# Kernel optimization log

Measured on AMD Instinct MI355X. Metric: run time of the kernel, lower is better.

Reference implementation:

```python
import jax, jax.numpy as jnp
import numpy as np

B, P, L1, D = 64, 16, 16, 1024  # images, people/img, object slots/img (slot0=no-object), feat dim
SP = 32   # flattened spatial (Conv_spatial output channels)
PROJ = 512
ACT = 29


def setup_inputs() -> dict:
    key = jax.random.key(0)
    ks = jax.random.split(key, 16)
    rn = lambda k, s, sc=1.0: jax.random.normal(k, s, dtype=jnp.float32) * sc
    w = 0.02  # weight init scale
    return {
        "people": rn(ks[0], (B, P, D)),
        "objects": rn(ks[1], (B, L1, D)),
        "context": rn(ks[2], (B, D)),
        "spatial": rn(ks[3], (B, P * L1, SP)),
        "Wvis_w": rn(ks[4], (3 * D, PROJ), w), "Wvis_b": jnp.zeros((PROJ,), jnp.float32),
        "Wspat_w": rn(ks[5], (SP, PROJ), w), "Wspat_b": jnp.zeros((PROJ,), jnp.float32),
        "Wip_w": rn(ks[6], (PROJ, 1), w), "Wip_b": jnp.zeros((1,), jnp.float32),
        "Wref_w": rn(ks[7], (PROJ, ACT), w), "Wref_b": jnp.zeros((ACT,), jnp.float32),
        "Watt_w": rn(ks[8], (PROJ, ACT), w), "Watt_b": jnp.zeros((ACT,), jnp.float32),
        "Woh_w": rn(ks[9], (D, D), w), "Woh_b": jnp.zeros((D,), jnp.float32),
        "Who_w": rn(ks[10], (D, D), w), "Who_b": jnp.zeros((D,), jnp.float32),
        "Wg_w": rn(ks[11], (2 * D, ACT), w), "Wg_b": jnp.zeros((ACT,), jnp.float32),
    }


def reference(people, objects, context, spatial,
              Wvis_w, Wvis_b, Wspat_w, Wspat_b, Wip_w, Wip_b,
              Wref_w, Wref_b, Watt_w, Watt_b,
              Woh_w, Woh_b, Who_w, Who_b, Wg_w, Wg_b):
    Bn, Pn, Dn = people.shape
    L = objects.shape[1]
    C = Bn * Pn * L

    # --- ROI.pairing: all (person, object-slot) pairs + image context -> [C, 3D]
    pe = jnp.broadcast_to(people[:, :, None, :], (Bn, Pn, L, Dn))
    ob = jnp.broadcast_to(objects[:, None, :, :], (Bn, Pn, L, Dn))
    cx = jnp.broadcast_to(context[:, None, None, :], (Bn, Pn, L, Dn))
    pairs = jnp.concatenate([pe, ob, cx], axis=-1).reshape(C, 3 * Dn)

    # --- attention / visual projection heads
    a_ho = jax.nn.relu(spatial.reshape(C, -1) @ Wspat_w + Wspat_b)   # W_Spat
    f_vis = jax.nn.relu(pairs @ Wvis_w + Wvis_b)                     # W_vis
    f_ref = f_vis * a_ho
    i_ho = f_ref @ Wip_w + Wip_b                                     # [C,1]
    interaction_prob = jax.nn.sigmoid(i_ho)
    p_ref = f_ref @ Wref_w + Wref_b                                  # [C,29]
    p_att = a_ho @ Watt_w + Watt_b                                   # [C,29]

    # --- graph message passing: adjacency = interaction probs, skipping slot 0 (no-object)
    adj = interaction_prob.reshape(Bn, Pn, L)[:, :, 1:]              # [B,P,O]
    oh = jax.nn.relu(objects[:, 1:] @ Woh_w + Woh_b)                 # W_oh on objects
    ho = jax.nn.relu(people @ Who_w + Who_b)                         # W_ho on people
    people_r = people + jnp.einsum('bpo,bod->bpd', adj, oh)
    objects_r = objects[:, 1:] + jnp.einsum('bpo,bpd->bod', adj, ho)
    objects_full = jnp.concatenate([objects[:, :1], objects_r], axis=1)  # re-attach no-object slot

    # --- refined all-pairs concat -> W_graph
    pe_r = jnp.broadcast_to(people_r[:, :, None, :], (Bn, Pn, L, Dn))
    ob_r = jnp.broadcast_to(objects_full[:, None, :, :], (Bn, Pn, L, Dn))
    pairs_g = jnp.concatenate([pe_r, ob_r], axis=-1).reshape(C, 2 * Dn)
    p_graph = pairs_g @ Wg_w + Wg_b                                  # [C,29]

    return (i_ho, p_ref, p_att, p_graph)
```

## Files before the change

kernel.cpp:

```cpp
#include <hip/hip_runtime.h>


typedef unsigned short u16;
typedef short s16x8 __attribute__((ext_vector_type(8)));
typedef float f32x4 __attribute__((ext_vector_type(4)));

__device__ __forceinline__ u16 f2b(float f) {
    union { float f; unsigned int i; } v; v.f = f;
    unsigned int r = (v.i + 0x7fffu + ((v.i >> 16) & 1u)) >> 16;
    return (u16)r;
}
__device__ __forceinline__ float b2f(u16 u) {
    union { float f; unsigned int i; } v; v.i = ((unsigned int)u) << 16; return v.f;
}
__device__ __forceinline__ unsigned int pack2(float x, float y) {
    return (unsigned int)f2b(x) | ((unsigned int)f2b(y) << 16);
}

#define OFF_WSPATT 0u
#define OFF_WREFT  32768u
#define OFF_WATTT  65536u
#define OFF_WGT    98304u
#define OFF_PP     229376u
#define OFF_PO     1277952u
#define OFF_PC     2326528u
#define OFF_ADJ    2392064u
#define OFF_HP     2457600u
#define OFF_HOF    2588672u
#define OFF_YH     2719744u
#define OFF_ZO     2850816u
#define ZERO_OFF   2457600u
#define ZERO_LEN   516096u
#define OFF_WVIST2 2973696u
#define OFF_WHOT2  6119424u
#define OFF_WOHT2  8216576u
#define OFF_PEOB   10313728u
#define OFF_OBJB   12410880u
#define OFF_CTXB   14508032u
#define OFF_SPATB  14639104u

__global__ __launch_bounds__(256) void prep_all(
    const float* __restrict__ people, const float* __restrict__ objects,
    const float* __restrict__ context, const float* __restrict__ spatial,
    const float* __restrict__ Wvis, const float* __restrict__ Who,
    const float* __restrict__ Woh, const float* __restrict__ Wspat,
    const float* __restrict__ Wref, const float* __restrict__ Watt,
    const float* __restrict__ Wg,
    u16* __restrict__ peoB, u16* __restrict__ objB, u16* __restrict__ ctxB,
    u16* __restrict__ spatB, u16* __restrict__ WvisT, u16* __restrict__ WhoT,
    u16* __restrict__ WohT, u16* __restrict__ WspatT, u16* __restrict__ WrefT,
    u16* __restrict__ WattT, u16* __restrict__ WgT)
{
    __shared__ float S[64][65];
    int bid = blockIdx.x, t = threadIdx.x;
    if (bid < 896) {
        const float* src; u16* dst; int N, K, kt, nt;
        int tb = bid;
        if (tb < 256)      { src = Who;  dst = WhoT;  K = 1024; N = 1024; kt = tb >> 4; nt = tb & 15; }
        else if (tb < 512) { tb -= 256; src = Woh;  dst = WohT;  K = 1024; N = 1024; kt = tb >> 4; nt = tb & 15; }
        else               { tb -= 512; src = Wvis; dst = WvisT; K = 3072; N = 512;  kt = tb >> 3; nt = tb & 7; }
        int k0 = kt * 64, n0 = nt * 64;
        int tx = t & 63, ty = t >> 6;
#pragma unroll
        for (int i = 0; i < 16; i++)
            S[ty + 4 * i][tx] = src[(size_t)(k0 + ty + 4 * i) * N + n0 + tx];
        __syncthreads();
#pragma unroll
        for (int i = 0; i < 16; i++)
            dst[(size_t)(n0 + ty + 4 * i) * K + k0 + tx] = f2b(S[tx][ty + 4 * i]);
        return;
    }
    int g = (bid - 896) * 256 + t;
    const int gsz = 512 * 256;
    for (int i = g; i < 524288; i += gsz) {
        float2 v = ((const float2*)people)[i];
        ((unsigned int*)peoB)[i] = pack2(v.x, v.y);
    }
    for (int i = g; i < 524288; i += gsz) {
        float2 v = ((const float2*)objects)[i];
        ((unsigned int*)objB)[i] = pack2(v.x, v.y);
    }
    for (int i = g; i < 32768; i += gsz) {
        float2 v = ((const float2*)context)[i];
        ((unsigned int*)ctxB)[i] = pack2(v.x, v.y);
    }
    for (int i = g; i < 262144; i += gsz) {
        float2 v = ((const float2*)spatial)[i];
        ((unsigned int*)spatB)[i] = pack2(v.x, v.y);
    }
    for (int i = g; i < 512 * 32; i += gsz) {
        int n = i >> 5, k = i & 31;
        WspatT[i] = f2b(Wspat[k * 512 + n]);
    }
    for (int i = g; i < 32 * 512; i += gsz) {
        int n = i >> 9, k = i & 511;
        WrefT[i] = (n < 29) ? f2b(Wref[k * 29 + n]) : (u16)0;
        WattT[i] = (n < 29) ? f2b(Watt[k * 29 + n]) : (u16)0;
    }
    for (int i = g; i < 32 * 2048; i += gsz) {
        int n = i >> 11, k = i & 2047;
        WgT[i] = (n < 29) ? f2b(Wg[k * 29 + n]) : (u16)0;
    }
}

__global__ __launch_bounds__(256) void fused_gemms(
    const u16* __restrict__ peoB, const u16* __restrict__ objB,
    const u16* __restrict__ ctxB, const u16* __restrict__ WvisT,
    const u16* __restrict__ WhoT, const float* __restrict__ Who_b,
    const u16* __restrict__ WohT, const float* __restrict__ Woh_b,
    const u16* __restrict__ WgT,
    u16* __restrict__ Pp, u16* __restrict__ Po, u16* __restrict__ Pc,
    float* __restrict__ Yh, float* __restrict__ Zo,
    float* __restrict__ Hp, float* __restrict__ HoF)
{
    __shared__ u16 T[128][72];
    int bid = blockIdx.x;
    int t = threadIdx.x;
    int lane = t & 63, w = t >> 6;
    int l16 = lane & 15, q = lane >> 4;
    int wy = w >> 1, wx = w & 1;

    if (bid < 264) {
        int bx = bid & 7, ty = bid >> 3;
        const u16* A; u16* outB; int koff, bm;
        if (ty < 16)      { A = peoB; outB = Pp; koff = 0;    bm = ty * 64; }
        else if (ty < 32) { A = objB; outB = Po; koff = 1024; bm = (ty - 16) * 64; }
        else              { A = ctxB; outB = Pc; koff = 2048; bm = 0; }
        int bn = bx * 64;

        const u16* ap0 = A + (size_t)(bm + wy * 32 + l16) * 1024 + q * 8;
        const u16* ap1 = ap0 + (size_t)16 * 1024;
        const u16* bp0 = WvisT + (size_t)(bn + wx * 32 + l16) * 3072 + koff + q * 8;
        const u16* bp1 = bp0 + (size_t)16 * 3072;

        f32x4 acc00 = {0,0,0,0}, acc01 = {0,0,0,0}, acc10 = {0,0,0,0}, acc11 = {0,0,0,0};
        s16x8 ca0 = *(const s16x8*)ap0,        ca1 = *(const s16x8*)ap1;
        s16x8 cb0 = *(const s16x8*)bp0,        cb1 = *(const s16x8*)bp1;
        s16x8 na0 = *(const s16x8*)(ap0 + 32), na1 = *(const s16x8*)(ap1 + 32);
        s16x8 nb0 = *(const s16x8*)(bp0 + 32), nb1 = *(const s16x8*)(bp1 + 32);
        ap0 += 64; ap1 += 64; bp0 += 64; bp1 += 64;
        for (int it = 0; it < 30; it++) {
            s16x8 ta0 = *(const s16x8*)ap0, ta1 = *(const s16x8*)ap1;
            s16x8 tb0 = *(const s16x8*)bp0, tb1 = *(const s16x8*)bp1;
            ap0 += 32; ap1 += 32; bp0 += 32; bp1 += 32;
            acc00 = __builtin_amdgcn_mfma_f32_16x16x32_bf16(ca0, cb0, acc00, 0, 0, 0);
            acc01 = __builtin_amdgcn_mfma_f32_16x16x32_bf16(ca0, cb1, acc01, 0, 0, 0);
            acc10 = __builtin_amdgcn_mfma_f32_16x16x32_bf16(ca1, cb0, acc10, 0, 0, 0);
            acc11 = __builtin_amdgcn_mfma_f32_16x16x32_bf16(ca1, cb1, acc11, 0, 0, 0);
            ca0 = na0; ca1 = na1; cb0 = nb0; cb1 = nb1;
            na0 = ta0; na1 = ta1; nb0 = tb0; nb1 = tb1;
        }
        acc00 = __builtin_amdgcn_mfma_f32_16x16x32_bf16(ca0, cb0, acc00, 0, 0, 0);
        acc01 = __builtin_amdgcn_mfma_f32_16x16x32_bf16(ca0, cb1, acc01, 0, 0, 0);
        acc10 = __builtin_amdgcn_mfma_f32_16x16x32_bf16(ca1, cb0, acc10, 0, 0, 0);
        acc11 = __builtin_amdgcn_mfma_f32_16x16x32_bf16(ca1, cb1, acc11, 0, 0, 0);
        acc00 = __builtin_amdgcn_mfma_f32_16x16x32_bf16(na0, nb0, acc00, 0, 0, 0);
        acc01 = __builtin_amdgcn_mfma_f32_16x16x32_bf16(na0, nb1, acc01, 0, 0, 0);
        acc10 = __builtin_amdgcn_mfma_f32_16x16x32_bf16(na1, nb0, acc10, 0, 0, 0);
        acc11 = __builtin_amdgcn_mfma_f32_16x16x32_bf16(na1, nb1, acc11, 0, 0, 0);

        f32x4 accs[2][2] = {{acc00, acc01}, {acc10, acc11}};
#pragma unroll
        for (int ii = 0; ii < 2; ii++)
#pragma unroll
            for (int jj = 0; jj < 2; jj++) {
                int col = bn + wx * 32 + jj * 16 + l16;
#pragma unroll
                for (int r = 0; r < 4; r++) {
                    int row = bm + wy * 32 + ii * 16 + q * 4 + r;
                    outB[(size_t)row * 512 + col] = f2b(accs[ii][jj][r]);
                }
            }
    } else if (bid < 520) {
        int r3 = bid - 264;
        int z = r3 >> 7; r3 &= 127;
        int rt = r3 >> 4, nbt = r3 & 15;
        const u16* A    = z ? objB : peoB;
        const u16* W1T  = z ? WohT : WhoT;
        const float* bb = z ? Woh_b : Who_b;
        const u16* Wg2  = z ? WgT : WgT + 1024;
        float* U        = z ? Zo : Yh;
        int m0 = rt * 128, nb = nbt * 64;

        const u16* ap[4];
        int rb = m0 + wy * 64;
#pragma unroll
        for (int i = 0; i < 4; i++) {
            int rr = rb + i * 16 + l16;
            if (z) { int rc = rr < 960 ? rr : 959; rr = (rc / 15) * 16 + (rc % 15) + 1; }
            ap[i] = A + (size_t)rr * 1024 + q * 8;
        }
        const u16* bp0 = W1T + (size_t)(nb + wx * 32 + l16) * 1024 + q * 8;
        const u16* bp1 = bp0 + (size_t)16 * 1024;

        f32x4 acc[4][2] = {};
        s16x8 ca[4], na[4];
#pragma unroll
        for (int i = 0; i < 4; i++) {
            ca[i] = *(const s16x8*)ap[i];
            na[i] = *(const s16x8*)(ap[i] + 32);
            ap[i] += 64;
        }
        s16x8 cb0 = *(const s16x8*)bp0, nb0 = *(const s16x8*)(bp0 + 32);
        s16x8 cb1 = *(const s16x8*)bp1, nb1 = *(const s16x8*)(bp1 + 32);
        bp0 += 64; bp1 += 64;
        for (int it = 0; it < 30; it++) {
            s16x8 ta[4], tb0, tb1;
#pragma unroll
            for (int i = 0; i < 4; i++) { ta[i] = *(const s16x8*)ap[i]; ap[i] += 32; }
            tb0 = *(const s16x8*)bp0; bp0 += 32;
            tb1 = *(const s16x8*)bp1; bp1 += 32;
#pragma unroll
            for (int i = 0; i < 4; i++) {
                acc[i][0] = __builtin_amdgcn_mfma_f32_16x16x32_bf16(ca[i], cb0, acc[i][0], 0, 0, 0);
                acc[i][1] = __builtin_amdgcn_mfma_f32_16x16x32_bf16(ca[i], cb1, acc[i][1], 0, 0, 0);
            }
#pragma unroll
            for (int i = 0; i < 4; i++) { ca[i] = na[i]; na[i] = ta[i]; }
            cb0 = nb0; nb0 = tb0; cb1 = nb1; nb1 = tb1;
        }
#pragma unroll
        for (int i = 0; i < 4; i++) {
            acc[i][0] = __builtin_amdgcn_mfma_f32_16x16x32_bf16(ca[i], cb0, acc[i][0], 0, 0, 0);
            acc[i][1] = __builtin_amdgcn_mfma_f32_16x16x32_bf16(ca[i], cb1, acc[i][1], 0, 0, 0);
        }
#pragma unroll
        for (int i = 0; i < 4; i++) {
            acc[i][0] = __builtin_amdgcn_mfma_f32_16x16x32_bf16(na[i], nb0, acc[i][0], 0, 0, 0);
            acc[i][1] = __builtin_amdgcn_mfma_f32_16x16x32_bf16(na[i], nb1, acc[i][1], 0, 0, 0);
        }

#pragma unroll
        for (int i = 0; i < 4; i++)
#pragma unroll
            for (int j = 0; j < 2; j++) {
                int col = wx * 32 + j * 16 + l16;
                float bv = bb[nb + col];
#pragma unroll
                for (int r = 0; r < 4; r++) {
                    float v = acc[i][j][r] + bv;
                    T[wy * 64 + i * 16 + q * 4 + r][col] = f2b(fmaxf(v, 0.f));
                }
            }
        __syncthreads();

        f32x4 s2[2][2] = {};
#pragma unroll
        for (int kk = 0; kk < 64; kk += 32) {
            s16x8 b20 = *(const s16x8*)(Wg2 + (size_t)l16 * 2048 + nb + kk + q * 8);
            s16x8 b21 = *(const s16x8*)(Wg2 + (size_t)(16 + l16) * 2048 + nb + kk + q * 8);
#pragma unroll
            for (int f = 0; f < 2; f++) {
                s16x8 a2 = *(const s16x8*)(&T[w * 32 + f * 16 + l16][kk + q * 8]);
                s2[f][0] = __builtin_amdgcn_mfma_f32_16x16x32_bf16(a2, b20, s2[f][0], 0, 0, 0);
                s2[f][1] = __builtin_amdgcn_mfma_f32_16x16x32_bf16(a2, b21, s2[f][1], 0, 0, 0);
            }
        }
#pragma unroll
        for (int f = 0; f < 2; f++)
#pragma unroll
            for (int r = 0; r < 4; r++) {
                int row = m0 + w * 32 + f * 16 + q * 4 + r;
                if (!z || row < 960) {
                    atomicAdd(&U[(size_t)row * 32 + l16], s2[f][0][r]);
                    atomicAdd(&U[(size_t)row * 32 + 16 + l16], s2[f][1][r]);
                }
            }
    } else {
        int r3 = bid - 520;
        int bx = r3 & 7, by = (r3 >> 3) & 7, z = r3 >> 6;
        const u16* A  = z ? objB : peoB;
        const u16* BT = z ? WgT + 1024 : WgT;
        float* outF   = z ? HoF : Hp;
        int bm = bx * 128 + w * 32;
        int kb = by * 128;
        const u16* ap0 = A + (size_t)(bm + l16) * 1024 + kb + q * 8;
        const u16* ap1 = A + (size_t)(bm + 16 + l16) * 1024 + kb + q * 8;
        const u16* bp0 = BT + (size_t)l16 * 2048 + kb + q * 8;
        const u16* bp1 = BT + (size_t)(16 + l16) * 2048 + kb + q * 8;
        f32x4 acc00 = {0,0,0,0}, acc01 = {0,0,0,0}, acc10 = {0,0,0,0}, acc11 = {0,0,0,0};
        s16x8 ca0 = *(const s16x8*)ap0,        ca1 = *(const s16x8*)ap1;
        s16x8 cb0 = *(const s16x8*)bp0,        cb1 = *(const s16x8*)bp1;
        s16x8 na0 = *(const s16x8*)(ap0 + 32), na1 = *(const s16x8*)(ap1 + 32);
        s16x8 nb0 = *(const s16x8*)(bp0 + 32), nb1 = *(const s16x8*)(bp1 + 32);
        ap0 += 64; ap1 += 64; bp0 += 64; bp1 += 64;
#pragma unroll
        for (int it = 0; it < 2; it++) {
            s16x8 ta0 = *(const s16x8*)ap0, ta1 = *(const s16x8*)ap1;
            s16x8 tb0 = *(const s16x8*)bp0, tb1 = *(const s16x8*)bp1;
            ap0 += 32; ap1 += 32; bp0 += 32; bp1 += 32;
            acc00 = __builtin_amdgcn_mfma_f32_16x16x32_bf16(ca0, cb0, acc00, 0, 0, 0);
            acc01 = __builtin_amdgcn_mfma_f32_16x16x32_bf16(ca0, cb1, acc01, 0, 0, 0);
            acc10 = __builtin_amdgcn_mfma_f32_16x16x32_bf16(ca1, cb0, acc10, 0, 0, 0);
            acc11 = __builtin_amdgcn_mfma_f32_16x16x32_bf16(ca1, cb1, acc11, 0, 0, 0);
            ca0 = na0; ca1 = na1; cb0 = nb0; cb1 = nb1;
            na0 = ta0; na1 = ta1; nb0 = tb0; nb1 = tb1;
        }
        acc00 = __builtin_amdgcn_mfma_f32_16x16x32_bf16(ca0, cb0, acc00, 0, 0, 0);
        acc01 = __builtin_amdgcn_mfma_f32_16x16x32_bf16(ca0, cb1, acc01, 0, 0, 0);
        acc10 = __builtin_amdgcn_mfma_f32_16x16x32_bf16(ca1, cb0, acc10, 0, 0, 0);
        acc11 = __builtin_amdgcn_mfma_f32_16x16x32_bf16(ca1, cb1, acc11, 0, 0, 0);
        acc00 = __builtin_amdgcn_mfma_f32_16x16x32_bf16(na0, nb0, acc00, 0, 0, 0);
        acc01 = __builtin_amdgcn_mfma_f32_16x16x32_bf16(na0, nb1, acc01, 0, 0, 0);
        acc10 = __builtin_amdgcn_mfma_f32_16x16x32_bf16(na1, nb0, acc10, 0, 0, 0);
        acc11 = __builtin_amdgcn_mfma_f32_16x16x32_bf16(na1, nb1, acc11, 0, 0, 0);
        f32x4 accs[2][2] = {{acc00, acc01}, {acc10, acc11}};
#pragma unroll
        for (int ii = 0; ii < 2; ii++)
#pragma unroll
            for (int jj = 0; jj < 2; jj++)
#pragma unroll
                for (int r = 0; r < 4; r++)
                    atomicAdd(&outF[(size_t)(bm + ii * 16 + q * 4 + r) * 32 + jj * 16 + l16],
                              accs[ii][jj][r]);
    }
}

__global__ __launch_bounds__(256) void mega(
    const u16* __restrict__ spatB, const u16* __restrict__ WspatT,
    const float* __restrict__ bspat,
    const u16* __restrict__ Pp, const u16* __restrict__ Po,
    const u16* __restrict__ Pc, const float* __restrict__ bvis,
    const u16* __restrict__ WrefT, const float* __restrict__ bref,
    const u16* __restrict__ WattT, const float* __restrict__ batt,
    const float* __restrict__ wip, const float* __restrict__ bip,
    float* __restrict__ outI, float* __restrict__ outRef,
    float* __restrict__ outAtt, float* __restrict__ adjw)
{
    __shared__ u16 tile[32][520];
    __shared__ float part[32][8];
    __shared__ float wipS[512];
    int t = threadIdx.x;
    int c0 = blockIdx.x * 32;
    int lane = t & 63, w = t >> 6;
    int l16 = lane & 15, q = lane >> 4;

    {
        float2 u = *(const float2*)(wip + t * 2);
        wipS[t * 2]     = u.x;
        wipS[t * 2 + 1] = u.y;
    }

    {
        s16x8 a0 = *(const s16x8*)(spatB + (size_t)(c0 + l16) * 32 + q * 8);
        s16x8 a1 = *(const s16x8*)(spatB + (size_t)(c0 + 16 + l16) * 32 + q * 8);
        const u16* wb = WspatT + (size_t)(w * 128 + l16) * 32 + q * 8;
        s16x8 cb = *(const s16x8*)wb;
        s16x8 nb_ = *(const s16x8*)(wb + 16 * 32);
        wb += 32 * 32;
#pragma unroll
        for (int nt = 0; nt < 8; nt++) {
            s16x8 tb = nb_;
            if (nt < 6) { tb = *(const s16x8*)wb; wb += 16 * 32; }
            int n = w * 128 + nt * 16;
            f32x4 acc0 = {0,0,0,0}, acc1 = {0,0,0,0};
            acc0 = __builtin_amdgcn_mfma_f32_16x16x32_bf16(a0, cb, acc0, 0, 0, 0);
            acc1 = __builtin_amdgcn_mfma_f32_16x16x32_bf16(a1, cb, acc1, 0, 0, 0);
            cb = nb_; nb_ = tb;
            float bias = bspat[n + l16];
#pragma unroll
            for (int r = 0; r < 4; r++) {
                tile[q * 4 + r][n + l16]      = f2b(fmaxf(acc0[r] + bias, 0.f));
                tile[16 + q * 4 + r][n + l16] = f2b(fmaxf(acc1[r] + bias, 0.f));
            }
        }
    }
    __syncthreads();

    {
        int rt = w >> 1, ct = w & 1;
        const u16* bp = WattT + (size_t)(ct * 16 + l16) * 512 + q * 8;
        f32x4 acc = {0,0,0,0};
        s16x8 cb = *(const s16x8*)bp;
        s16x8 nb_ = *(const s16x8*)(bp + 32);
        bp += 64;
        for (int i = 0; i < 14; i++) {
            s16x8 tb = *(const s16x8*)bp; bp += 32;
            s16x8 a = *(const s16x8*)(&tile[rt * 16 + l16][i * 32 + q * 8]);
            acc = __builtin_amdgcn_mfma_f32_16x16x32_bf16(a, cb, acc, 0, 0, 0);
            cb = nb_; nb_ = tb;
        }
        {
            s16x8 a = *(const s16x8*)(&tile[rt * 16 + l16][14 * 32 + q * 8]);
            acc = __builtin_amdgcn_mfma_f32_16x16x32_bf16(a, cb, acc, 0, 0, 0);
            a = *(const s16x8*)(&tile[rt * 16 + l16][15 * 32 + q * 8]);
            acc = __builtin_amdgcn_mfma_f32_16x16x32_bf16(a, nb_, acc, 0, 0, 0);
        }
        int col = ct * 16 + l16;
        if (col < 29) {
            float bias = batt[col];
#pragma unroll
            for (int r = 0; r < 4; r++) {
                int row = c0 + rt * 16 + q * 4 + r;
                outAtt[(size_t)row * 29 + col] = acc[r] + bias;
            }
        }
    }
    __syncthreads();

    {
        int row = t >> 3, g = t & 7;
        int c = c0 + row;
        int rp = c >> 4, bimg = c >> 8;
        int ro = bimg * 16 + (c & 15);
        const u16* ppr = Pp + (size_t)rp * 512;
        const u16* por = Po + (size_t)ro * 512;
        const u16* pcr = Pc + (size_t)bimg * 512;
        float ps = 0.f;
#pragma unroll 4
        for (int j = 0; j < 64; j += 2) {
            int col = g * 64 + j;
            unsigned int upp = *(const unsigned int*)(ppr + col);
            unsigned int upo = *(const unsigned int*)(por + col);
            unsigned int upc = *(const unsigned int*)(pcr + col);
            float2 bv = *(const float2*)(bvis + col);
            unsigned int uah = *(const unsigned int*)(&tile[row][col]);
            float fv0 = fmaxf(b2f((u16)(upp & 0xffff)) + b2f((u16)(upo & 0xffff))
                            + b2f((u16)(upc & 0xffff)) + bv.x, 0.f);
            float fv1 = fmaxf(b2f((u16)(upp >> 16)) + b2f((u16)(upo >> 16))
                            + b2f((u16)(upc >> 16)) + bv.y, 0.f);
            float fr0 = fv0 * b2f((u16)(uah & 0xffff));
            float fr1 = fv1 * b2f((u16)(uah >> 16));
            *(unsigned int*)(&tile[row][col]) = pack2(fr0, fr1);
            ps += fr0 * wipS[col] + fr1 * wipS[col + 1];
        }
        part[row][g] = ps;
    }
    __syncthreads();

    if (t < 32) {
        float s = part[t][0] + part[t][1] + part[t][2] + part[t][3]
                + part[t][4] + part[t][5] + part[t][6] + part[t][7] + bip[0];
        outI[c0 + t] = s;
        adjw[c0 + t] = 1.f / (1.f + expf(-s));
    }

    {
        int rt = w >> 1, ct = w & 1;
        const u16* bp = WrefT + (size_t)(ct * 16 + l16) * 512 + q * 8;
        f32x4 acc = {0,0,0,0};
        s16x8 cb = *(const s16x8*)bp;
        s16x8 nb_ = *(const s16x8*)(bp + 32);
        bp += 64;
        for (int i = 0; i < 14; i++) {
            s16x8 tb = *(const s16x8*)bp; bp += 32;
            s16x8 a = *(const s16x8*)(&tile[rt * 16 + l16][i * 32 + q * 8]);
            acc = __builtin_amdgcn_mfma_f32_16x16x32_bf16(a, cb, acc, 0, 0, 0);
            cb = nb_; nb_ = tb;
        }
        {
            s16x8 a = *(const s16x8*)(&tile[rt * 16 + l16][14 * 32 + q * 8]);
            acc = __builtin_amdgcn_mfma_f32_16x16x32_bf16(a, cb, acc, 0, 0, 0);
            a = *(const s16x8*)(&tile[rt * 16 + l16][15 * 32 + q * 8]);
            acc = __builtin_amdgcn_mfma_f32_16x16x32_bf16(a, nb_, acc, 0, 0, 0);
        }
        int col = ct * 16 + l16;
        if (col < 29) {
            float bias = bref[col];
#pragma unroll
            for (int r = 0; r < 4; r++) {
                int row = c0 + rt * 16 + q * 4 + r;
                outRef[(size_t)row * 29 + col] = acc[r] + bias;
            }
        }
    }
}

__global__ __launch_bounds__(256) void pgraph2(
    const float* __restrict__ adjw, const float* __restrict__ Hp,
    const float* __restrict__ HoF, const float* __restrict__ Yh,
    const float* __restrict__ Zo, const float* __restrict__ bg,
    float* __restrict__ outG)
{
    int b = blockIdx.x, t = threadIdx.x;
    __shared__ float adjS[16][16];
    __shared__ float YhS[16][32];
    __shared__ float ZoS[15][32];
    __shared__ float PA[16][32];
    __shared__ float OA[16][32];
    adjS[t >> 4][t & 15] = adjw[b * 256 + t];
    for (int i = t; i < 512; i += 256)
        YhS[i >> 5][i & 31] = Yh[(size_t)(b * 16 + (i >> 5)) * 32 + (i & 31)];
    for (int i = t; i < 480; i += 256)
        ZoS[i >> 5][i & 31] = Zo[(size_t)(b * 15 + (i >> 5)) * 32 + (i & 31)];
    __syncthreads();
    for (int i = t; i < 512; i += 256) {
        int p = i >> 5, j = i & 31;
        float s = 0.f;
#pragma unroll
        for (int o = 0; o < 15; o++) s += adjS[p][o + 1] * ZoS[o][j];
        PA[p][j] = s;
        float s2 = 0.f;
#pragma unroll
        for (int pp = 0; pp < 16; pp++) s2 += adjS[pp][p] * YhS[pp][j];
        OA[p][j] = s2;
    }
    __syncthreads();
    int p = t >> 4, l = t & 15;
    const float* hp = Hp + (size_t)(b * 16 + p) * 32;
    const float* ho = HoF + (size_t)(b * 16 + l) * 32;
    size_t c = (size_t)b * 256 + t;
    for (int j = 0; j < 29; j++) {
        float v = hp[j] + ho[j] + bg[j] + PA[p][j];
        if (l >= 1) v += OA[l][j];
        outG[c * 29 + j] = v;
    }
}

extern "C" void kernel_launch(void* const* d_in, const int* in_sizes, int n_in,
                              void* d_out, int out_size, void* d_ws, size_t ws_size,
                              hipStream_t stream)
{
    const float* people  = (const float*)d_in[0];
    const float* objects = (const float*)d_in[1];
    const float* context = (const float*)d_in[2];
    const float* spatial = (const float*)d_in[3];
    const float* Wvis_w  = (const float*)d_in[4];
    const float* Wvis_b  = (const float*)d_in[5];
    const float* Wspat_w = (const float*)d_in[6];
    const float* Wspat_b = (const float*)d_in[7];
    const float* Wip_w   = (const float*)d_in[8];
    const float* Wip_b   = (const float*)d_in[9];
    const float* Wref_w  = (const float*)d_in[10];
    const float* Wref_b  = (const float*)d_in[11];
    const float* Watt_w  = (const float*)d_in[12];
    const float* Watt_b  = (const float*)d_in[13];
    const float* Woh_w   = (const float*)d_in[14];
    const float* Woh_b   = (const float*)d_in[15];
    const float* Who_w   = (const float*)d_in[16];
    const float* Who_b   = (const float*)d_in[17];
    const float* Wg_w    = (const float*)d_in[18];
    const float* Wg_b    = (const float*)d_in[19];

    char* ws = (char*)d_ws;
    u16* WspatT = (u16*)(ws + OFF_WSPATT);
    u16* WrefT  = (u16*)(ws + OFF_WREFT);
    u16* WattT  = (u16*)(ws + OFF_WATTT);
    u16* WgT    = (u16*)(ws + OFF_WGT);
    u16* Ppb    = (u16*)(ws + OFF_PP);
    u16* Pob    = (u16*)(ws + OFF_PO);
    u16* Pcb    = (u16*)(ws + OFF_PC);
    float* adjw = (float*)(ws + OFF_ADJ);
    float* Hp   = (float*)(ws + OFF_HP);
    float* HoF  = (float*)(ws + OFF_HOF);
    float* Yh   = (float*)(ws + OFF_YH);
    float* Zo   = (float*)(ws + OFF_ZO);
    u16* WvisT2 = (u16*)(ws + OFF_WVIST2);
    u16* WhoT2  = (u16*)(ws + OFF_WHOT2);
    u16* WohT2  = (u16*)(ws + OFF_WOHT2);
    u16* peoB   = (u16*)(ws + OFF_PEOB);
    u16* objB   = (u16*)(ws + OFF_OBJB);
    u16* ctxB   = (u16*)(ws + OFF_CTXB);
    u16* spatB  = (u16*)(ws + OFF_SPATB);

    float* outI   = (float*)d_out;
    float* outRef = outI + 16384;
    float* outAtt = outI + 491520;
    float* outG   = outI + 966656;

    hipMemsetAsync(ws + ZERO_OFF, 0, ZERO_LEN, stream);

    prep_all<<<1408, 256, 0, stream>>>(people, objects, context, spatial,
        Wvis_w, Who_w, Woh_w, Wspat_w, Wref_w, Watt_w, Wg_w,
        peoB, objB, ctxB, spatB, WvisT2, WhoT2, WohT2,
        WspatT, WrefT, WattT, WgT);

    fused_gemms<<<648, 256, 0, stream>>>(peoB, objB, ctxB, WvisT2,
        WhoT2, Who_b, WohT2, Woh_b, WgT,
        Ppb, Pob, Pcb, Yh, Zo, Hp, HoF);

    mega<<<512, 256, 0, stream>>>(spatB, WspatT, Wspat_b,
                                  Ppb, Pob, Pcb, Wvis_b,
                                  WrefT, Wref_b, WattT, Watt_b,
                                  Wip_w, Wip_b,
                                  outI, outRef, outAtt, adjw);

    pgraph2<<<64, 256, 0, stream>>>(adjw, Hp, HoF, Yh, Zo, Wg_b, outG);
}
```

Before: 189.6 us.

## Split-K visual projection with fp32 atomics and halve mega block rows

The visual projection GEMM for people, objects and context is split into two K halves. Each half accumulates into fp32 partial buffers with atomicAdd, which doubles the block count in that phase; the buffers are zeroed by an extra memset. The mega kernel now handles 16 pair rows per block instead of 32, giving twice as many blocks, but only two of its four waves do the att/ref MFMA work. The consumer now reads fp32 partials, which doubles that read traffic compared with bf16, and the atomics add contention and nondeterministic summation order.

```diff
diff --git a/kernel.cpp b/kernel.cpp
--- a/kernel.cpp
+++ b/kernel.cpp
@@ -21,9 +21,6 @@
 #define OFF_WREFT  32768u
 #define OFF_WATTT  65536u
 #define OFF_WGT    98304u
-#define OFF_PP     229376u
-#define OFF_PO     1277952u
-#define OFF_PC     2326528u
 #define OFF_ADJ    2392064u
 #define OFF_HP     2457600u
 #define OFF_HOF    2588672u
@@ -38,6 +35,11 @@
 #define OFF_OBJB   12410880u
 #define OFF_CTXB   14508032u
 #define OFF_SPATB  14639104u
+#define OFF_PPF    15687680u
+#define OFF_POF    17784832u
+#define OFF_PCF    19881984u
+#define ZERO2_OFF  15687680u
+#define ZERO2_LEN  4325376u
 
 __global__ __launch_bounds__(256) void prep_all(
     const float* __restrict__ people, const float* __restrict__ objects,
@@ -109,7 +111,7 @@
     const u16* __restrict__ WhoT, const float* __restrict__ Who_b,
     const u16* __restrict__ WohT, const float* __restrict__ Woh_b,
     const u16* __restrict__ WgT,
-    u16* __restrict__ Pp, u16* __restrict__ Po, u16* __restrict__ Pc,
+    float* __restrict__ PpF, float* __restrict__ PoF, float* __restrict__ PcF,
     float* __restrict__ Yh, float* __restrict__ Zo,
     float* __restrict__ Hp, float* __restrict__ HoF)
 {
@@ -120,17 +122,20 @@
     int l16 = lane & 15, q = lane >> 4;
     int wy = w >> 1, wx = w & 1;
 
-    if (bid < 264) {
-        int bx = bid & 7, ty = bid >> 3;
-        const u16* A; u16* outB; int koff, bm;
-        if (ty < 16)      { A = peoB; outB = Pp; koff = 0;    bm = ty * 64; }
-        else if (ty < 32) { A = objB; outB = Po; koff = 1024; bm = (ty - 16) * 64; }
-        else              { A = ctxB; outB = Pc; koff = 2048; bm = 0; }
+    if (bid < 528) {
+        int ks = bid >= 264;
+        int sub = bid - ks * 264;
+        int bx = sub & 7, ty = sub >> 3;
+        const u16* A; float* outF; int koff, bm;
+        if (ty < 16)      { A = peoB; outF = PpF; koff = 0;    bm = ty * 64; }
+        else if (ty < 32) { A = objB; outF = PoF; koff = 1024; bm = (ty - 16) * 64; }
+        else              { A = ctxB; outF = PcF; koff = 2048; bm = 0; }
         int bn = bx * 64;
-
-        const u16* ap0 = A + (size_t)(bm + wy * 32 + l16) * 1024 + q * 8;
+        int k0 = ks * 512;
+
+        const u16* ap0 = A + (size_t)(bm + wy * 32 + l16) * 1024 + k0 + q * 8;
         const u16* ap1 = ap0 + (size_t)16 * 1024;
-        const u16* bp0 = WvisT + (size_t)(bn + wx * 32 + l16) * 3072 + koff + q * 8;
+        const u16* bp0 = WvisT + (size_t)(bn + wx * 32 + l16) * 3072 + koff + k0 + q * 8;
         const u16* bp1 = bp0 + (size_t)16 * 3072;
 
         f32x4 acc00 = {0,0,0,0}, acc01 = {0,0,0,0}, acc10 = {0,0,0,0}, acc11 = {0,0,0,0};
@@ -139,7 +144,7 @@
         s16x8 na0 = *(const s16x8*)(ap0 + 32), na1 = *(const s16x8*)(ap1 + 32);
         s16x8 nb0 = *(const s16x8*)(bp0 + 32), nb1 = *(const s16x8*)(bp1 + 32);
         ap0 += 64; ap1 += 64; bp0 += 64; bp1 += 64;
-        for (int it = 0; it < 30; it++) {
+        for (int it = 0; it < 14; it++) {
             s16x8 ta0 = *(const s16x8*)ap0, ta1 = *(const s16x8*)ap1;
             s16x8 tb0 = *(const s16x8*)bp0, tb1 = *(const s16x8*)bp1;
             ap0 += 32; ap1 += 32; bp0 += 32; bp1 += 32;
@@ -168,11 +173,11 @@
 #pragma unroll
                 for (int r = 0; r < 4; r++) {
                     int row = bm + wy * 32 + ii * 16 + q * 4 + r;
-                    outB[(size_t)row * 512 + col] = f2b(accs[ii][jj][r]);
+                    atomicAdd(&outF[(size_t)row * 512 + col], accs[ii][jj][r]);
                 }
             }
-    } else if (bid < 520) {
-        int r3 = bid - 264;
+    } else if (bid < 784) {
+        int r3 = bid - 528;
         int z = r3 >> 7; r3 &= 127;
         int rt = r3 >> 4, nbt = r3 & 15;
         const u16* A    = z ? objB : peoB;
@@ -267,7 +272,7 @@
                 }
             }
     } else {
-        int r3 = bid - 520;
+        int r3 = bid - 784;
         int bx = r3 & 7, by = (r3 >> 3) & 7, z = r3 >> 6;
         const u16* A  = z ? objB : peoB;
         const u16* BT = z ? WgT + 1024 : WgT;
@@ -319,19 +324,19 @@
 __global__ __launch_bounds__(256) void mega(
     const u16* __restrict__ spatB, const u16* __restrict__ WspatT,
     const float* __restrict__ bspat,
-    const u16* __restrict__ Pp, const u16* __restrict__ Po,
-    const u16* __restrict__ Pc, const float* __restrict__ bvis,
+    const float* __restrict__ PpF, const float* __restrict__ PoF,
+    const float* __restrict__ PcF, const float* __restrict__ bvis,
     const u16* __restrict__ WrefT, const float* __restrict__ bref,
     const u16* __restrict__ WattT, const float* __restrict__ batt,
     const float* __restrict__ wip, const float* __restrict__ bip,
     float* __restrict__ outI, float* __restrict__ outRef,
     float* __restrict__ outAtt, float* __restrict__ adjw)
 {
-    __shared__ u16 tile[32][520];
-    __shared__ float part[32][8];
+    __shared__ u16 tile[16][520];
+    __shared__ float part[16][16];
     __shared__ float wipS[512];
     int t = threadIdx.x;
-    int c0 = blockIdx.x * 32;
+    int c0 = blockIdx.x * 16;
     int lane = t & 63, w = t >> 6;
     int l16 = lane & 15, q = lane >> 4;
 
@@ -343,7 +348,6 @@
 
     {
         s16x8 a0 = *(const s16x8*)(spatB + (size_t)(c0 + l16) * 32 + q * 8);
-        s16x8 a1 = *(const s16x8*)(spatB + (size_t)(c0 + 16 + l16) * 32 + q * 8);
         const u16* wb = WspatT + (size_t)(w * 128 + l16) * 32 + q * 8;
         s16x8 cb = *(const s16x8*)wb;
         s16x8 nb_ = *(const s16x8*)(wb + 16 * 32);
@@ -353,22 +357,19 @@
             s16x8 tb = nb_;
             if (nt < 6) { tb = *(const s16x8*)wb; wb += 16 * 32; }
             int n = w * 128 + nt * 16;
-            f32x4 acc0 = {0,0,0,0}, acc1 = {0,0,0,0};
+            f32x4 acc0 = {0,0,0,0};
             acc0 = __builtin_amdgcn_mfma_f32_16x16x32_bf16(a0, cb, acc0, 0, 0, 0);
-            acc1 = __builtin_amdgcn_mfma_f32_16x16x32_bf16(a1, cb, acc1, 0, 0, 0);
             cb = nb_; nb_ = tb;
             float bias = bspat[n + l16];
 #pragma unroll
-            for (int r = 0; r < 4; r++) {
-                tile[q * 4 + r][n + l16]      = f2b(fmaxf(acc0[r] + bias, 0.f));
-                tile[16 + q * 4 + r][n + l16] = f2b(fmaxf(acc1[r] + bias, 0.f));
-            }
+            for (int r = 0; r < 4; r++)
+                tile[q * 4 + r][n + l16] = f2b(fmaxf(acc0[r] + bias, 0.f));
         }
     }
     __syncthreads();
 
-    {
-        int rt = w >> 1, ct = w & 1;
+    if (w < 2) {
+        int ct = w;
         const u16* bp = WattT + (size_t)(ct * 16 + l16) * 512 + q * 8;
         f32x4 acc = {0,0,0,0};
         s16x8 cb = *(const s16x8*)bp;
@@ -376,14 +377,14 @@
         bp += 64;
         for (int i = 0; i < 14; i++) {
             s16x8 tb = *(const s16x8*)bp; bp += 32;
-            s16x8 a = *(const s16x8*)(&tile[rt * 16 + l16][i * 32 + q * 8]);
+            s16x8 a = *(const s16x8*)(&tile[l16][i * 32 + q * 8]);
             acc = __builtin_amdgcn_mfma_f32_16x16x32_bf16(a, cb, acc, 0, 0, 0);
             cb = nb_; nb_ = tb;
         }
         {
-            s16x8 a = *(const s16x8*)(&tile[rt * 16 + l16][14 * 32 + q * 8]);
+            s16x8 a = *(const s16x8*)(&tile[l16][14 * 32 + q * 8]);
             acc = __builtin_amdgcn_mfma_f32_16x16x32_bf16(a, cb, acc, 0, 0, 0);
-            a = *(const s16x8*)(&tile[rt * 16 + l16][15 * 32 + q * 8]);
+            a = *(const s16x8*)(&tile[l16][15 * 32 + q * 8]);
             acc = __builtin_amdgcn_mfma_f32_16x16x32_bf16(a, nb_, acc, 0, 0, 0);
         }
         int col = ct * 16 + l16;
@@ -391,7 +392,7 @@
             float bias = batt[col];
 #pragma unroll
             for (int r = 0; r < 4; r++) {
-                int row = c0 + rt * 16 + q * 4 + r;
+                int row = c0 + q * 4 + r;
                 outAtt[(size_t)row * 29 + col] = acc[r] + bias;
             }
         }
@@ -399,26 +400,24 @@
     __syncthreads();
 
     {
-        int row = t >> 3, g = t & 7;
+        int row = t >> 4, g = t & 15;
         int c = c0 + row;
         int rp = c >> 4, bimg = c >> 8;
         int ro = bimg * 16 + (c & 15);
-        const u16* ppr = Pp + (size_t)rp * 512;
-        const u16* por = Po + (size_t)ro * 512;
-        const u16* pcr = Pc + (size_t)bimg * 512;
+        const float* ppr = PpF + (size_t)rp * 512;
+        const float* por = PoF + (size_t)ro * 512;
+        const float* pcr = PcF + (size_t)bimg * 512;
         float ps = 0.f;
 #pragma unroll 4
-        for (int j = 0; j < 64; j += 2) {
-            int col = g * 64 + j;
-            unsigned int upp = *(const unsigned int*)(ppr + col);
-            unsigned int upo = *(const unsigned int*)(por + col);
-            unsigned int upc = *(const unsigned int*)(pcr + col);
+        for (int j = 0; j < 32; j += 2) {
+            int col = g * 32 + j;
+            float2 pp = *(const float2*)(ppr + col);
+            float2 po = *(const float2*)(por + col);
+            float2 pc = *(const float2*)(pcr + col);
             float2 bv = *(const float2*)(bvis + col);
             unsigned int uah = *(const unsigned int*)(&tile[row][col]);
-            float fv0 = fmaxf(b2f((u16)(upp & 0xffff)) + b2f((u16)(upo & 0xffff))
-                            + b2f((u16)(upc & 0xffff)) + bv.x, 0.f);
-            float fv1 = fmaxf(b2f((u16)(upp >> 16)) + b2f((u16)(upo >> 16))
-                            + b2f((u16)(upc >> 16)) + bv.y, 0.f);
+            float fv0 = fmaxf(pp.x + po.x + pc.x + bv.x, 0.f);
+            float fv1 = fmaxf(pp.y + po.y + pc.y + bv.y, 0.f);
             float fr0 = fv0 * b2f((u16)(uah & 0xffff));
             float fr1 = fv1 * b2f((u16)(uah >> 16));
             *(unsigned int*)(&tile[row][col]) = pack2(fr0, fr1);
@@ -428,15 +427,16 @@
     }
     __syncthreads();
 
-    if (t < 32) {
-        float s = part[t][0] + part[t][1] + part[t][2] + part[t][3]
-                + part[t][4] + part[t][5] + part[t][6] + part[t][7] + bip[0];
+    if (t < 16) {
+        float s = bip[0];
+#pragma unroll
+        for (int i = 0; i < 16; i++) s += part[t][i];
         outI[c0 + t] = s;
         adjw[c0 + t] = 1.f / (1.f + expf(-s));
     }
 
-    {
-        int rt = w >> 1, ct = w & 1;
+    if (w < 2) {
+        int ct = w;
         const u16* bp = WrefT + (size_t)(ct * 16 + l16) * 512 + q * 8;
         f32x4 acc = {0,0,0,0};
         s16x8 cb = *(const s16x8*)bp;
@@ -444,14 +444,14 @@
         bp += 64;
         for (int i = 0; i < 14; i++) {
             s16x8 tb = *(const s16x8*)bp; bp += 32;
-            s16x8 a = *(const s16x8*)(&tile[rt * 16 + l16][i * 32 + q * 8]);
+            s16x8 a = *(const s16x8*)(&tile[l16][i * 32 + q * 8]);
             acc = __builtin_amdgcn_mfma_f32_16x16x32_bf16(a, cb, acc, 0, 0, 0);
             cb = nb_; nb_ = tb;
         }
         {
-            s16x8 a = *(const s16x8*)(&tile[rt * 16 + l16][14 * 32 + q * 8]);
+            s16x8 a = *(const s16x8*)(&tile[l16][14 * 32 + q * 8]);
             acc = __builtin_amdgcn_mfma_f32_16x16x32_bf16(a, cb, acc, 0, 0, 0);
-            a = *(const s16x8*)(&tile[rt * 16 + l16][15 * 32 + q * 8]);
+            a = *(const s16x8*)(&tile[l16][15 * 32 + q * 8]);
             acc = __builtin_amdgcn_mfma_f32_16x16x32_bf16(a, nb_, acc, 0, 0, 0);
         }
         int col = ct * 16 + l16;
@@ -459,7 +459,7 @@
             float bias = bref[col];
 #pragma unroll
             for (int r = 0; r < 4; r++) {
-                int row = c0 + rt * 16 + q * 4 + r;
+                int row = c0 + q * 4 + r;
                 outRef[(size_t)row * 29 + col] = acc[r] + bias;
             }
         }
@@ -537,9 +537,6 @@
     u16* WrefT  = (u16*)(ws + OFF_WREFT);
     u16* WattT  = (u16*)(ws + OFF_WATTT);
     u16* WgT    = (u16*)(ws + OFF_WGT);
-    u16* Ppb    = (u16*)(ws + OFF_PP);
-    u16* Pob    = (u16*)(ws + OFF_PO);
-    u16* Pcb    = (u16*)(ws + OFF_PC);
     float* adjw = (float*)(ws + OFF_ADJ);
     float* Hp   = (float*)(ws + OFF_HP);
     float* HoF  = (float*)(ws + OFF_HOF);
@@ -552,6 +549,9 @@
     u16* objB   = (u16*)(ws + OFF_OBJB);
     u16* ctxB   = (u16*)(ws + OFF_CTXB);
     u16* spatB  = (u16*)(ws + OFF_SPATB);
+    float* PpF  = (float*)(ws + OFF_PPF);
+    float* PoF  = (float*)(ws + OFF_POF);
+    float* PcF  = (float*)(ws + OFF_PCF);
 
     float* outI   = (float*)d_out;
     float* outRef = outI + 16384;
@@ -559,21 +559,22 @@
     float* outG   = outI + 966656;
 
     hipMemsetAsync(ws + ZERO_OFF, 0, ZERO_LEN, stream);
+    hipMemsetAsync(ws + ZERO2_OFF, 0, ZERO2_LEN, stream);
 
     prep_all<<<1408, 256, 0, stream>>>(people, objects, context, spatial,
         Wvis_w, Who_w, Woh_w, Wspat_w, Wref_w, Watt_w, Wg_w,
         peoB, objB, ctxB, spatB, WvisT2, WhoT2, WohT2,
         WspatT, WrefT, WattT, WgT);
 
-    fused_gemms<<<648, 256, 0, stream>>>(peoB, objB, ctxB, WvisT2,
+    fused_gemms<<<912, 256, 0, stream>>>(peoB, objB, ctxB, WvisT2,
         WhoT2, Who_b, WohT2, Woh_b, WgT,
-        Ppb, Pob, Pcb, Yh, Zo, Hp, HoF);
-
-    mega<<<512, 256, 0, stream>>>(spatB, WspatT, Wspat_b,
-                                  Ppb, Pob, Pcb, Wvis_b,
-                                  WrefT, Wref_b, WattT, Watt_b,
-                                  Wip_w, Wip_b,
-                                  outI, outRef, outAtt, adjw);
+        PpF, PoF, PcF, Yh, Zo, Hp, HoF);
+
+    mega<<<1024, 256, 0, stream>>>(spatB, WspatT, Wspat_b,
+                                   PpF, PoF, PcF, Wvis_b,
+                                   WrefT, Wref_b, WattT, Watt_b,
+                                   Wip_w, Wip_b,
+                                   outI, outRef, outAtt, adjw);
 
     pgraph2<<<64, 256, 0, stream>>>(adjw, Hp, HoF, Yh, Zo, Wg_b, outG);
 }
```

After: 207.7 us. 9.5% more time.
